# Optimization experiments

Hardware: AMD Instinct MI355X
Metric: run time of the kernel (lower is better)

## Reference

```python
import jax, jax.numpy as jnp
import numpy as np

N = 131072      # total nodes in batch
D = 128         # input_dim
K_EXP = 1024    # input_dim * num_conv_kernels
H = 512         # cluster_model_hidden_dim
NG = 4          # number of groups (sub-models)
F_SEG = 8192    # fine clusters (global_max_pool segments)
G_SEG = 32      # coarse graphs (InstanceNorm segments)
C = 16          # node_num_classes
EPS = 1e-5      # InstanceNorm eps


def setup_inputs() -> dict:
    key = jax.random.key(0)
    ks = jax.random.split(key, 8)
    x = jax.random.normal(ks[0], (N, D), jnp.float32)
    # disjoint partition of node indices into NG groups (gather/scatter dispatch)
    group_indices = jax.random.permutation(ks[1], N).reshape(NG, N // NG)
    # sorted segment ids, every segment non-empty
    pool_cluster_fine = (jnp.arange(N) // (N // F_SEG)).astype(jnp.int32)
    batch_cluster_coarse = (jnp.arange(F_SEG) // (F_SEG // G_SEG)).astype(jnp.int32)
    # per-group NodeModel params: expand D -> K_EXP, relu, project -> H
    W1 = jax.random.normal(ks[2], (NG, D, K_EXP), jnp.float32) * (1.0 / np.sqrt(D))
    b1 = jnp.zeros((NG, K_EXP), jnp.float32)
    W2 = jax.random.normal(ks[3], (NG, K_EXP, H), jnp.float32) * (1.0 / np.sqrt(K_EXP))
    b2 = jnp.zeros((NG, H), jnp.float32)
    # classifier (glorot weight, zero bias)
    w_out = jax.random.normal(ks[4], (H, C), jnp.float32) * np.sqrt(2.0 / (H + C))
    b_out = jnp.zeros((C,), jnp.float32)
    return {"x": x, "group_indices": group_indices,
            "pool_cluster_fine": pool_cluster_fine,
            "batch_cluster_coarse": batch_cluster_coarse,
            "W1": W1, "b1": b1, "W2": W2, "b2": b2,
            "w_out": w_out, "b_out": b_out}


def reference(x, group_indices, pool_cluster_fine, batch_cluster_coarse,
              W1, b1, W2, b2, w_out, b_out):
    # per-group gather -> sub-model -> scatter (vectorized over groups)
    xg = x[group_indices]                                   # [NG, N/NG, D]
    h = jax.nn.relu(jnp.einsum('gnd,gdk->gnk', xg, W1) + b1[:, None, :])
    og = jnp.einsum('gnk,gkh->gnh', h, W2) + b2[:, None, :]  # [NG, N/NG, H]
    new_feat = jnp.zeros((x.shape[0], H), x.dtype).at[group_indices.reshape(-1)].set(
        og.reshape(-1, H))                                   # [N, H]
    # global_max_pool over fine clusters
    emb = jax.ops.segment_max(new_feat, pool_cluster_fine,
                              num_segments=F_SEG, indices_are_sorted=True)  # [F, H]
    # PyG InstanceNorm(affine=False): per coarse-graph, per-channel standardization
    ones = jnp.ones((F_SEG, 1), emb.dtype)
    cnt = jax.ops.segment_sum(ones, batch_cluster_coarse,
                              num_segments=G_SEG, indices_are_sorted=True)  # [G,1]
    mean = jax.ops.segment_sum(emb, batch_cluster_coarse,
                               num_segments=G_SEG, indices_are_sorted=True) / cnt
    var = jax.ops.segment_sum(emb * emb, batch_cluster_coarse,
                              num_segments=G_SEG, indices_are_sorted=True) / cnt - mean ** 2
    normed = (emb - mean[batch_cluster_coarse]) * jax.lax.rsqrt(var[batch_cluster_coarse] + EPS)
    # dropout is identity in eval mode; classifier
    logits = normed @ w_out + b_out                          # [F, C]
    return logits
```

## Files before the change

kernel.cpp:

```cpp
#include <hip/hip_runtime.h>
#include <stdint.h>

typedef __bf16 bf16;
typedef bf16 bf16x8 __attribute__((ext_vector_type(8)));
typedef float f32x4 __attribute__((ext_vector_type(4)));

#define N_NODES 131072
#define D_IN    128
#define KEXP    1024
#define H_DIM   512
#define NGRP    4
#define NPG     32768
#define F_SEG   8192
#define G_SEG   32
#define C_OUT   16

typedef const __attribute__((address_space(1))) void* gas_t;
typedef __attribute__((address_space(3))) void* las_t;
__device__ __forceinline__ void cp16_async(const bf16* g, bf16* l) {
    __builtin_amdgcn_global_load_lds((gas_t)g, (las_t)l, 16, 0, 0);
}

__global__ void convert_weights(const float* __restrict__ W1,
                                const float* __restrict__ W2,
                                bf16* __restrict__ W1F,
                                bf16* __restrict__ W2F)
{
    int t = blockIdx.x * 256 + threadIdx.x;
    if (t < 65536) {
        int slot = t & 63, f = (t >> 6) & 7, kc = (t >> 9) & 31, g = t >> 14;
        int ks = f >> 1, nt = f & 1, quad = slot >> 4, ln = slot & 15;
        int k = kc * 32 + nt * 16 + ln;
        const float* src = W1 + ((size_t)(g * 128 + ks * 32 + quad * 8)) * 1024 + k;
        bf16x8 v;
        #pragma unroll
        for (int j = 0; j < 8; ++j) v[j] = (bf16)src[(size_t)j * 1024];
        *(bf16x8*)(W1F + (size_t)t * 8) = v;
    } else {
        int u = t - 65536;
        if (u < 262144) {
            int slot = u & 63, f = (u >> 6) & 15, kc = (u >> 10) & 31;
            int n0t2 = (u >> 15) & 1, g = u >> 16;
            int quad = slot >> 4, ln = slot & 15;
            int k = kc * 32 + quad * 8;
            int n = n0t2 * 256 + f * 16 + ln;
            const float* src = W2 + ((size_t)(g * 1024 + k)) * 512 + n;
            bf16x8 v;
            #pragma unroll
            for (int j = 0; j < 8; ++j) v[j] = (bf16)src[(size_t)j * 512];
            *(bf16x8*)(W2F + (size_t)u * 8) = v;
        }
    }
}

__global__ __launch_bounds__(256, 2)
void mlp_kernel(const float* __restrict__ x,
                const int*   __restrict__ gidx,
                const bf16*  __restrict__ W1F,
                const float* __restrict__ b1,
                const bf16*  __restrict__ W2F,
                const float* __restrict__ b2,
                bf16*        __restrict__ NF)
{
    __shared__ __align__(16) bf16 sW1[2][4096];
    __shared__ __align__(16) bf16 sW2[2][8192];
    __shared__ __align__(16) bf16 sH[4096];

    const int tid  = threadIdx.x;
    const int bid  = blockIdx.x;
    const int g    = bid >> 9;
    const int rem  = bid & 511;
    const int m0   = (rem >> 1) * 128;
    const int n0t2 = rem & 1;

    const int wave = tid >> 6;
    const int lane = tid & 63;
    const int quad = lane >> 4;
    const int ln   = lane & 15;

    const int*  gI  = gidx + g * NPG + m0;
    const bf16* W1g = W1F + (size_t)g * 131072;
    const bf16* W2g = W2F + (size_t)(g * 2 + n0t2) * 262144;
    const float* b1g = b1 + g * KEXP;
    const float* b2g = b2 + g * H_DIM + n0t2 * 256;

    bf16x8 xf[8];
    #pragma unroll
    for (int i = 0; i < 8; ++i) {
        int row  = wave * 32 + (i >> 2) * 16 + ln;
        int node = gI[row];
        const float* src = x + (size_t)node * D_IN + (i & 3) * 32 + quad * 8;
        float4 a = *(const float4*)src;
        float4 b = *(const float4*)(src + 4);
        bf16x8 v;
        v[0] = (bf16)a.x; v[1] = (bf16)a.y; v[2] = (bf16)a.z; v[3] = (bf16)a.w;
        v[4] = (bf16)b.x; v[5] = (bf16)b.y; v[6] = (bf16)b.z; v[7] = (bf16)b.w;
        xf[i] = v;
    }

    f32x4 acc2[2][16];
    #pragma unroll
    for (int a = 0; a < 2; ++a)
        #pragma unroll
        for (int b = 0; b < 16; ++b)
            acc2[a][b] = (f32x4){0.f, 0.f, 0.f, 0.f};

    #pragma unroll
    for (int r = 0; r < 2; ++r) {
        int c = r * 4 + wave;
        cp16_async(W1g + c * 512 + lane * 8, sW1[0] + c * 512);
    }
    #pragma unroll
    for (int r = 0; r < 4; ++r) {
        int c = r * 4 + wave;
        cp16_async(W2g + c * 512 + lane * 8, sW2[0] + c * 512);
    }

    #pragma unroll 1
    for (int kc = 0; kc < 32; ++kc) {
        __syncthreads();

        {
            int nkc = (kc + 1) & 31;
            const bf16* w1src = W1g + (size_t)nkc * 4096;
            const bf16* w2src = W2g + (size_t)nkc * 8192;
            bf16* d1 = sW1[(kc + 1) & 1];
            bf16* d2 = sW2[(kc + 1) & 1];
            #pragma unroll
            for (int r = 0; r < 2; ++r) {
                int c = r * 4 + wave;
                cp16_async(w1src + c * 512 + lane * 8, d1 + c * 512);
            }
            #pragma unroll
            for (int r = 0; r < 4; ++r) {
                int c = r * 4 + wave;
                cp16_async(w2src + c * 512 + lane * 8, d2 + c * 512);
            }
        }
        const bf16* w1buf = sW1[kc & 1];
        const bf16* w2buf = sW2[kc & 1];

        float bias_v[2];
        #pragma unroll
        for (int nt = 0; nt < 2; ++nt)
            bias_v[nt] = b1g[kc * 32 + nt * 16 + ln];

        f32x4 acc1[2][2];
        #pragma unroll
        for (int a = 0; a < 2; ++a)
            #pragma unroll
            for (int b = 0; b < 2; ++b)
                acc1[a][b] = (f32x4){0.f, 0.f, 0.f, 0.f};

        #pragma unroll
        for (int ks = 0; ks < 4; ++ks) {
            #pragma unroll
            for (int nt = 0; nt < 2; ++nt) {
                bf16x8 bfr = *(const bf16x8*)(w1buf + ((ks * 2 + nt) * 64 + lane) * 8);
                #pragma unroll
                for (int mt = 0; mt < 2; ++mt)
                    acc1[mt][nt] = __builtin_amdgcn_mfma_f32_16x16x32_bf16(
                        xf[mt * 4 + ks], bfr, acc1[mt][nt], 0, 0, 0);
            }
        }

        #pragma unroll
        for (int nt = 0; nt < 2; ++nt) {
            float bias = bias_v[nt];
            int base = wave * 1024 + (nt * 2 + (ln >> 3)) * 128
                     + (quad * 4) * 8 + (ln & 7);
            #pragma unroll
            for (int mt = 0; mt < 2; ++mt) {
                int fb = base + mt * 512;
                #pragma unroll
                for (int reg = 0; reg < 4; ++reg) {
                    float v = acc1[mt][nt][reg] + bias;
                    sH[fb + reg * 8] = (bf16)fmaxf(v, 0.f);
                }
            }
        }

        bf16x8 a2[2];
        #pragma unroll
        for (int mt = 0; mt < 2; ++mt)
            a2[mt] = *(const bf16x8*)(sH + wave * 1024 + mt * 512 + lane * 8);
        #pragma unroll
        for (int nt = 0; nt < 16; ++nt) {
            bf16x8 bb = *(const bf16x8*)(w2buf + (nt * 64 + lane) * 8);
            #pragma unroll
            for (int mt = 0; mt < 2; ++mt)
                acc2[mt][nt] = __builtin_amdgcn_mfma_f32_16x16x32_bf16(
                    a2[mt], bb, acc2[mt][nt], 0, 0, 0);
        }
    }

    float b2v[16];
    #pragma unroll
    for (int nt = 0; nt < 16; ++nt) b2v[nt] = b2g[nt * 16 + ln];

    #pragma unroll
    for (int mt = 0; mt < 2; ++mt)
        #pragma unroll
        for (int reg = 0; reg < 4; ++reg) {
            int row  = wave * 32 + mt * 16 + quad * 4 + reg;
            int node = gI[row];
            bf16* dst = NF + (size_t)node * H_DIM + n0t2 * 256;
            #pragma unroll
            for (int nt = 0; nt < 16; ++nt)
                dst[nt * 16 + ln] = (bf16)(acc2[mt][nt][reg] + b2v[nt]);
        }
}

__global__ void pool_kernel(const bf16* __restrict__ NF, float* __restrict__ EMB)
{
    int t  = blockIdx.x * 256 + threadIdx.x;
    int f  = t >> 8;
    int hp = (t & 255) * 2;
    const uint32_t* src = (const uint32_t*)NF;
    size_t base = (size_t)f * 4096 + (hp >> 1);
    float lo = -INFINITY, hi = -INFINITY;
    #pragma unroll
    for (int r = 0; r < 16; ++r) {
        uint32_t v = src[base + (size_t)r * 256];
        lo = fmaxf(lo, __uint_as_float(v << 16));
        hi = fmaxf(hi, __uint_as_float(v & 0xffff0000u));
    }
    *(float2*)(EMB + (size_t)f * 512 + hp) = make_float2(lo, hi);
}

__global__ void stats_kernel(const float* __restrict__ EMB,
                             float* __restrict__ MEAN,
                             float* __restrict__ RSIG)
{
    int gc = blockIdx.x;
    int ch = blockIdx.y * 128 + threadIdx.x;
    const float* p = EMB + (size_t)gc * 256 * 512 + ch;
    float s = 0.f, ss = 0.f;
    #pragma unroll 4
    for (int r = 0; r < 256; ++r) {
        float v = p[(size_t)r * 512];
        s += v; ss += v * v;
    }
    float mean = s * (1.f / 256.f);
    float var  = ss * (1.f / 256.f) - mean * mean;
    MEAN[gc * 512 + ch] = mean;
    RSIG[gc * 512 + ch] = rsqrtf(var + 1e-5f);
}

__global__ __launch_bounds__(256)
void classifier_kernel(const float* __restrict__ EMB,
                       const float* __restrict__ MEAN,
                       const float* __restrict__ RSIG,
                       const float* __restrict__ w_out,
                       const float* __restrict__ b_out,
                       float* __restrict__ out)
{
    __shared__ float sW[512 * 16];
    __shared__ float sE[16 * 513];
    int t  = threadIdx.x;
    int f0 = blockIdx.x * 16;
    int gc = f0 >> 8;

    #pragma unroll
    for (int it = 0; it < 8; ++it) {
        int i = (it * 256 + t) * 4;
        *(float4*)(sW + i) = *(const float4*)(w_out + i);
    }
    #pragma unroll
    for (int it = 0; it < 32; ++it) {
        int i  = it * 256 + t;
        int fr = i >> 9;
        int h  = i & 511;
        float v = EMB[(size_t)(f0 + fr) * 512 + h];
        sE[fr * 513 + h] = (v - MEAN[gc * 512 + h]) * RSIG[gc * 512 + h];
    }
    __syncthreads();

    int fr = t >> 4;
    int c  = t & 15;
    float acc = b_out[c];
    #pragma unroll 8
    for (int h = 0; h < 512; ++h)
        acc += sE[fr * 513 + h] * sW[h * 16 + c];
    out[(size_t)(f0 + fr) * 16 + c] = acc;
}

extern "C" void kernel_launch(void* const* d_in, const int* in_sizes, int n_in,
                              void* d_out, int out_size, void* d_ws, size_t ws_size,
                              hipStream_t stream)
{
    const float* x     = (const float*)d_in[0];
    const int*   gidx  = (const int*)d_in[1];
    const float* W1    = (const float*)d_in[4];
    const float* b1    = (const float*)d_in[5];
    const float* W2    = (const float*)d_in[6];
    const float* b2    = (const float*)d_in[7];
    const float* w_out = (const float*)d_in[8];
    const float* b_out = (const float*)d_in[9];
    float* out = (float*)d_out;

    char* w = (char*)d_ws;
    bf16* W1F = (bf16*)w;  w += (size_t)NGRP * KEXP * D_IN * 2;
    bf16* W2F = (bf16*)w;  w += (size_t)NGRP * H_DIM * KEXP * 2;
    bf16* NF  = (bf16*)w;  w += (size_t)N_NODES * H_DIM * 2;
    float* EMB  = (float*)w; w += (size_t)F_SEG * H_DIM * 4;
    float* MEAN = (float*)w; w += (size_t)G_SEG * H_DIM * 4;
    float* RSIG = (float*)w; w += (size_t)G_SEG * H_DIM * 4;

    convert_weights<<<1280, 256, 0, stream>>>(W1, W2, W1F, W2F);
    mlp_kernel<<<2048, 256, 0, stream>>>(x, gidx, W1F, b1, W2F, b2, NF);
    pool_kernel<<<8192, 256, 0, stream>>>(NF, EMB);
    stats_kernel<<<dim3(32, 4), 128, 0, stream>>>(EMB, MEAN, RSIG);
    classifier_kernel<<<512, 256, 0, stream>>>(EMB, MEAN, RSIG, w_out, b_out, out);
}
```

Baseline: 387.5 us.

## Fuse segment max-pool into MLP epilogue via atomicMax on order-preserving encoded floats

Removes the bf16 NF intermediate and the separate pool kernel. The MLP epilogue now does atomicMax directly into an fp32 embedding buffer, using a sign-flipping float-to-uint encoding so integer max matches float max. The embedding buffer is zeroed inside the weight-conversion kernel. The second GEMM is also re-tiled so each wave covers all 128 rows against its own 64 output columns, with an extra barrier because sH is now shared across waves. This trades a large NF write and re-read for many global atomics (16 nodes per segment hit the same address) and an added sync per k-step.

```diff
diff --git a/kernel.cpp b/kernel.cpp
--- a/kernel.cpp
+++ b/kernel.cpp
@@ -21,10 +21,20 @@
     __builtin_amdgcn_global_load_lds((gas_t)g, (las_t)l, 16, 0, 0);
 }
 
+__device__ __forceinline__ uint32_t enc_f32(float f) {
+    uint32_t b = __float_as_uint(f);
+    return (b & 0x80000000u) ? ~b : (b | 0x80000000u);
+}
+__device__ __forceinline__ float dec_f32(uint32_t k) {
+    uint32_t b = (k & 0x80000000u) ? (k & 0x7FFFFFFFu) : ~k;
+    return __uint_as_float(b);
+}
+
 __global__ void convert_weights(const float* __restrict__ W1,
                                 const float* __restrict__ W2,
                                 bf16* __restrict__ W1F,
-                                bf16* __restrict__ W2F)
+                                bf16* __restrict__ W2F,
+                                uint32_t* __restrict__ EMBu)
 {
     int t = blockIdx.x * 256 + threadIdx.x;
     if (t < 65536) {
@@ -36,20 +46,21 @@
         #pragma unroll
         for (int j = 0; j < 8; ++j) v[j] = (bf16)src[(size_t)j * 1024];
         *(bf16x8*)(W1F + (size_t)t * 8) = v;
+    } else if (t < 327680) {
+        int u = t - 65536;
+        int slot = u & 63, f = (u >> 6) & 15, kc = (u >> 10) & 31;
+        int n0t2 = (u >> 15) & 1, g = u >> 16;
+        int quad = slot >> 4, ln = slot & 15;
+        int k = kc * 32 + quad * 8;
+        int n = n0t2 * 256 + f * 16 + ln;
+        const float* src = W2 + ((size_t)(g * 1024 + k)) * 512 + n;
+        bf16x8 v;
+        #pragma unroll
+        for (int j = 0; j < 8; ++j) v[j] = (bf16)src[(size_t)j * 512];
+        *(bf16x8*)(W2F + (size_t)u * 8) = v;
     } else {
-        int u = t - 65536;
-        if (u < 262144) {
-            int slot = u & 63, f = (u >> 6) & 15, kc = (u >> 10) & 31;
-            int n0t2 = (u >> 15) & 1, g = u >> 16;
-            int quad = slot >> 4, ln = slot & 15;
-            int k = kc * 32 + quad * 8;
-            int n = n0t2 * 256 + f * 16 + ln;
-            const float* src = W2 + ((size_t)(g * 1024 + k)) * 512 + n;
-            bf16x8 v;
-            #pragma unroll
-            for (int j = 0; j < 8; ++j) v[j] = (bf16)src[(size_t)j * 512];
-            *(bf16x8*)(W2F + (size_t)u * 8) = v;
-        }
+        int z = t - 327680;
+        if (z < F_SEG * H_DIM) EMBu[z] = 0u;
     }
 }
 
@@ -60,7 +71,7 @@
                 const float* __restrict__ b1,
                 const bf16*  __restrict__ W2F,
                 const float* __restrict__ b2,
-                bf16*        __restrict__ NF)
+                uint32_t*    __restrict__ EMBu)
 {
     __shared__ __align__(16) bf16 sW1[2][4096];
     __shared__ __align__(16) bf16 sW2[2][8192];
@@ -98,11 +109,11 @@
         xf[i] = v;
     }
 
-    f32x4 acc2[2][16];
-    #pragma unroll
-    for (int a = 0; a < 2; ++a)
-        #pragma unroll
-        for (int b = 0; b < 16; ++b)
+    f32x4 acc2[8][4];
+    #pragma unroll
+    for (int a = 0; a < 8; ++a)
+        #pragma unroll
+        for (int b = 0; b < 4; ++b)
             acc2[a][b] = (f32x4){0.f, 0.f, 0.f, 0.f};
 
     #pragma unroll
@@ -120,26 +131,7 @@
     for (int kc = 0; kc < 32; ++kc) {
         __syncthreads();
 
-        {
-            int nkc = (kc + 1) & 31;
-            const bf16* w1src = W1g + (size_t)nkc * 4096;
-            const bf16* w2src = W2g + (size_t)nkc * 8192;
-            bf16* d1 = sW1[(kc + 1) & 1];
-            bf16* d2 = sW2[(kc + 1) & 1];
-            #pragma unroll
-            for (int r = 0; r < 2; ++r) {
-                int c = r * 4 + wave;
-                cp16_async(w1src + c * 512 + lane * 8, d1 + c * 512);
-            }
-            #pragma unroll
-            for (int r = 0; r < 4; ++r) {
-                int c = r * 4 + wave;
-                cp16_async(w2src + c * 512 + lane * 8, d2 + c * 512);
-            }
-        }
         const bf16* w1buf = sW1[kc & 1];
-        const bf16* w2buf = sW2[kc & 1];
-
         float bias_v[2];
         #pragma unroll
         for (int nt = 0; nt < 2; ++nt)
@@ -168,7 +160,7 @@
         for (int nt = 0; nt < 2; ++nt) {
             float bias = bias_v[nt];
             int base = wave * 1024 + (nt * 2 + (ln >> 3)) * 128
-                     + (quad * 4) * 8 + (ln & 7);
+                     + quad * 32 + (ln & 7);
             #pragma unroll
             for (int mt = 0; mt < 2; ++mt) {
                 int fb = base + mt * 512;
@@ -180,65 +172,72 @@
             }
         }
 
-        bf16x8 a2[2];
-        #pragma unroll
-        for (int mt = 0; mt < 2; ++mt)
-            a2[mt] = *(const bf16x8*)(sH + wave * 1024 + mt * 512 + lane * 8);
-        #pragma unroll
-        for (int nt = 0; nt < 16; ++nt) {
-            bf16x8 bb = *(const bf16x8*)(w2buf + (nt * 64 + lane) * 8);
-            #pragma unroll
-            for (int mt = 0; mt < 2; ++mt)
+        __syncthreads();
+
+        {
+            int nkc = (kc + 1) & 31;
+            const bf16* w1src = W1g + (size_t)nkc * 4096;
+            const bf16* w2src = W2g + (size_t)nkc * 8192;
+            bf16* d1 = sW1[(kc + 1) & 1];
+            bf16* d2 = sW2[(kc + 1) & 1];
+            #pragma unroll
+            for (int r = 0; r < 2; ++r) {
+                int c = r * 4 + wave;
+                cp16_async(w1src + c * 512 + lane * 8, d1 + c * 512);
+            }
+            #pragma unroll
+            for (int r = 0; r < 4; ++r) {
+                int c = r * 4 + wave;
+                cp16_async(w2src + c * 512 + lane * 8, d2 + c * 512);
+            }
+        }
+
+        const bf16* w2buf = sW2[kc & 1];
+        bf16x8 bb[4];
+        #pragma unroll
+        for (int nt = 0; nt < 4; ++nt)
+            bb[nt] = *(const bf16x8*)(w2buf + ((wave * 4 + nt) * 64 + lane) * 8);
+        #pragma unroll
+        for (int mt = 0; mt < 8; ++mt) {
+            bf16x8 a2 = *(const bf16x8*)(sH + (mt * 64 + lane) * 8);
+            #pragma unroll
+            for (int nt = 0; nt < 4; ++nt)
                 acc2[mt][nt] = __builtin_amdgcn_mfma_f32_16x16x32_bf16(
-                    a2[mt], bb, acc2[mt][nt], 0, 0, 0);
-        }
-    }
-
-    float b2v[16];
-    #pragma unroll
-    for (int nt = 0; nt < 16; ++nt) b2v[nt] = b2g[nt * 16 + ln];
-
-    #pragma unroll
-    for (int mt = 0; mt < 2; ++mt)
+                    a2, bb[nt], acc2[mt][nt], 0, 0, 0);
+        }
+    }
+
+    float b2v[4];
+    #pragma unroll
+    for (int nt = 0; nt < 4; ++nt) b2v[nt] = b2g[wave * 64 + nt * 16 + ln];
+
+    #pragma unroll
+    for (int mt = 0; mt < 8; ++mt)
         #pragma unroll
         for (int reg = 0; reg < 4; ++reg) {
-            int row  = wave * 32 + mt * 16 + quad * 4 + reg;
+            int row  = mt * 16 + quad * 4 + reg;
             int node = gI[row];
-            bf16* dst = NF + (size_t)node * H_DIM + n0t2 * 256;
-            #pragma unroll
-            for (int nt = 0; nt < 16; ++nt)
-                dst[nt * 16 + ln] = (bf16)(acc2[mt][nt][reg] + b2v[nt]);
-        }
-}
-
-__global__ void pool_kernel(const bf16* __restrict__ NF, float* __restrict__ EMB)
-{
-    int t  = blockIdx.x * 256 + threadIdx.x;
-    int f  = t >> 8;
-    int hp = (t & 255) * 2;
-    const uint32_t* src = (const uint32_t*)NF;
-    size_t base = (size_t)f * 4096 + (hp >> 1);
-    float lo = -INFINITY, hi = -INFINITY;
-    #pragma unroll
-    for (int r = 0; r < 16; ++r) {
-        uint32_t v = src[base + (size_t)r * 256];
-        lo = fmaxf(lo, __uint_as_float(v << 16));
-        hi = fmaxf(hi, __uint_as_float(v & 0xffff0000u));
-    }
-    *(float2*)(EMB + (size_t)f * 512 + hp) = make_float2(lo, hi);
-}
-
-__global__ void stats_kernel(const float* __restrict__ EMB,
+            uint32_t* dst = EMBu + (size_t)(node >> 4) * H_DIM
+                          + n0t2 * 256 + wave * 64;
+            #pragma unroll
+            for (int nt = 0; nt < 4; ++nt) {
+                float v = acc2[mt][nt][reg] + b2v[nt];
+                atomicMax(dst + nt * 16 + ln, enc_f32(v));
+            }
+        }
+}
+
+__global__ void stats_kernel(const uint32_t* __restrict__ EMBu,
                              float* __restrict__ MEAN,
                              float* __restrict__ RSIG)
 {
     int gc = blockIdx.x;
     int ch = blockIdx.y * 128 + threadIdx.x;
-    const float* p = EMB + (size_t)gc * 256 * 512 + ch;
+    const uint32_t* p = EMBu + (size_t)gc * 256 * 512 + ch;
     float s = 0.f, ss = 0.f;
     #pragma unroll 4
     for (int r = 0; r < 256; ++r) {
-        float v = p[(size_t)r * 512];
+        float v = dec_f32(p[(size_t)r * 512]);
         s += v; ss += v * v;
     }
     float mean = s * (1.f / 256.f);
@@ -248,7 +247,7 @@
 }
 
 __global__ __launch_bounds__(256)
-void classifier_kernel(const float* __restrict__ EMB,
+void classifier_kernel(const uint32_t* __restrict__ EMBu,
                        const float* __restrict__ MEAN,
                        const float* __restrict__ RSIG,
                        const float* __restrict__ w_out,
@@ -271,7 +270,7 @@
         int i  = it * 256 + t;
         int fr = i >> 9;
         int h  = i & 511;
-        float v = EMB[(size_t)(f0 + fr) * 512 + h];
+        float v = dec_f32(EMBu[(size_t)(f0 + fr) * 512 + h]);
         sE[fr * 513 + h] = (v - MEAN[gc * 512 + h]) * RSIG[gc * 512 + h];
     }
     __syncthreads();
@@ -302,14 +301,12 @@
     char* w = (char*)d_ws;
     bf16* W1F = (bf16*)w;  w += (size_t)NGRP * KEXP * D_IN * 2;
     bf16* W2F = (bf16*)w;  w += (size_t)NGRP * H_DIM * KEXP * 2;
-    bf16* NF  = (bf16*)w;  w += (size_t)N_NODES * H_DIM * 2;
-    float* EMB  = (float*)w; w += (size_t)F_SEG * H_DIM * 4;
+    uint32_t* EMBu = (uint32_t*)w; w += (size_t)F_SEG * H_DIM * 4;
     float* MEAN = (float*)w; w += (size_t)G_SEG * H_DIM * 4;
     float* RSIG = (float*)w; w += (size_t)G_SEG * H_DIM * 4;
 
-    convert_weights<<<1280, 256, 0, stream>>>(W1, W2, W1F, W2F);
-    mlp_kernel<<<2048, 256, 0, stream>>>(x, gidx, W1F, b1, W2F, b2, NF);
-    pool_kernel<<<8192, 256, 0, stream>>>(NF, EMB);
-    stats_kernel<<<dim3(32, 4), 128, 0, stream>>>(EMB, MEAN, RSIG);
-    classifier_kernel<<<512, 256, 0, stream>>>(EMB, MEAN, RSIG, w_out, b_out, out);
-}
+    convert_weights<<<17664, 256, 0, stream>>>(W1, W2, W1F, W2F, EMBu);
+    mlp_kernel<<<2048, 256, 0, stream>>>(x, gidx, W1F, b1, W2F, b2, EMBu);
+    stats_kernel<<<dim3(32, 4), 128, 0, stream>>>(EMBu, MEAN, RSIG);
+    classifier_kernel<<<512, 256, 0, stream>>>(EMBu, MEAN, RSIG, w_out, b_out, out);
+}
```

Result: slower. 446.3 us (+15.2%).

## Retile second GEMM as 2x2 wave grid and vectorize max-pool loads

Applied to the files above, without the earlier changes.

The second GEMM in the MLP kernel is re-tiled so each wave computes a 64x128 output tile (4 M-tiles by 8 N-tiles) instead of 32x256. Every wave now reads the shared hidden activations written by the other waves, so a barrier is added after the sH writes, and the W1 prefetch is moved after that barrier so it cannot overwrite buffers still being read. The point is to cut LDS traffic for W2 fragments per MFMA, at the cost of an extra barrier per k-chunk and different register pressure. Separately, the pool kernel loads 16-byte vectors of 8 bf16 channels per thread and launches a quarter as many blocks.

```diff
diff --git a/kernel.cpp b/kernel.cpp
--- a/kernel.cpp
+++ b/kernel.cpp
@@ -77,12 +77,13 @@
     const int lane = tid & 63;
     const int quad = lane >> 4;
     const int ln   = lane & 15;
+    const int mg   = wave >> 1;
+    const int ng   = wave & 1;
 
     const int*  gI  = gidx + g * NPG + m0;
     const bf16* W1g = W1F + (size_t)g * 131072;
     const bf16* W2g = W2F + (size_t)(g * 2 + n0t2) * 262144;
     const float* b1g = b1 + g * KEXP;
-    const float* b2g = b2 + g * H_DIM + n0t2 * 256;
 
     bf16x8 xf[8];
     #pragma unroll
@@ -98,11 +99,11 @@
         xf[i] = v;
     }
 
-    f32x4 acc2[2][16];
-    #pragma unroll
-    for (int a = 0; a < 2; ++a)
-        #pragma unroll
-        for (int b = 0; b < 16; ++b)
+    f32x4 acc2[4][8];
+    #pragma unroll
+    for (int a = 0; a < 4; ++a)
+        #pragma unroll
+        for (int b = 0; b < 8; ++b)
             acc2[a][b] = (f32x4){0.f, 0.f, 0.f, 0.f};
 
     #pragma unroll
@@ -122,24 +123,16 @@
 
         {
             int nkc = (kc + 1) & 31;
-            const bf16* w1src = W1g + (size_t)nkc * 4096;
             const bf16* w2src = W2g + (size_t)nkc * 8192;
-            bf16* d1 = sW1[(kc + 1) & 1];
             bf16* d2 = sW2[(kc + 1) & 1];
-            #pragma unroll
-            for (int r = 0; r < 2; ++r) {
-                int c = r * 4 + wave;
-                cp16_async(w1src + c * 512 + lane * 8, d1 + c * 512);
-            }
             #pragma unroll
             for (int r = 0; r < 4; ++r) {
                 int c = r * 4 + wave;
                 cp16_async(w2src + c * 512 + lane * 8, d2 + c * 512);
             }
         }
+
         const bf16* w1buf = sW1[kc & 1];
-        const bf16* w2buf = sW2[kc & 1];
-
         float bias_v[2];
         #pragma unroll
         for (int nt = 0; nt < 2; ++nt)
@@ -168,7 +161,7 @@
         for (int nt = 0; nt < 2; ++nt) {
             float bias = bias_v[nt];
             int base = wave * 1024 + (nt * 2 + (ln >> 3)) * 128
-                     + (quad * 4) * 8 + (ln & 7);
+                     + quad * 32 + (ln & 7);
             #pragma unroll
             for (int mt = 0; mt < 2; ++mt) {
                 int fb = base + mt * 512;
@@ -180,33 +173,48 @@
             }
         }
 
-        bf16x8 a2[2];
-        #pragma unroll
-        for (int mt = 0; mt < 2; ++mt)
-            a2[mt] = *(const bf16x8*)(sH + wave * 1024 + mt * 512 + lane * 8);
-        #pragma unroll
-        for (int nt = 0; nt < 16; ++nt) {
-            bf16x8 bb = *(const bf16x8*)(w2buf + (nt * 64 + lane) * 8);
-            #pragma unroll
-            for (int mt = 0; mt < 2; ++mt)
+        __syncthreads();
+
+        {
+            int nkc = (kc + 1) & 31;
+            const bf16* w1src = W1g + (size_t)nkc * 4096;
+            bf16* d1 = sW1[(kc + 1) & 1];
+            #pragma unroll
+            for (int r = 0; r < 2; ++r) {
+                int c = r * 4 + wave;
+                cp16_async(w1src + c * 512 + lane * 8, d1 + c * 512);
+            }
+        }
+
+        const bf16* w2buf = sW2[kc & 1];
+        bf16x8 bb[8];
+        #pragma unroll
+        for (int nt = 0; nt < 8; ++nt)
+            bb[nt] = *(const bf16x8*)(w2buf + ((ng * 8 + nt) * 64 + lane) * 8);
+        #pragma unroll
+        for (int mt = 0; mt < 4; ++mt) {
+            bf16x8 a2 = *(const bf16x8*)(sH + ((mg * 4 + mt) * 64 + lane) * 8);
+            #pragma unroll
+            for (int nt = 0; nt < 8; ++nt)
                 acc2[mt][nt] = __builtin_amdgcn_mfma_f32_16x16x32_bf16(
-                    a2[mt], bb, acc2[mt][nt], 0, 0, 0);
-        }
-    }
-
-    float b2v[16];
-    #pragma unroll
-    for (int nt = 0; nt < 16; ++nt) b2v[nt] = b2g[nt * 16 + ln];
-
-    #pragma unroll
-    for (int mt = 0; mt < 2; ++mt)
+                    a2, bb[nt], acc2[mt][nt], 0, 0, 0);
+        }
+    }
+
+    const float* b2g = b2 + g * H_DIM + n0t2 * 256 + ng * 128;
+    float b2v[8];
+    #pragma unroll
+    for (int nt = 0; nt < 8; ++nt) b2v[nt] = b2g[nt * 16 + ln];
+
+    #pragma unroll
+    for (int mt = 0; mt < 4; ++mt)
         #pragma unroll
         for (int reg = 0; reg < 4; ++reg) {
-            int row  = wave * 32 + mt * 16 + quad * 4 + reg;
+            int row  = mg * 64 + mt * 16 + quad * 4 + reg;
             int node = gI[row];
-            bf16* dst = NF + (size_t)node * H_DIM + n0t2 * 256;
-            #pragma unroll
-            for (int nt = 0; nt < 16; ++nt)
+            bf16* dst = NF + (size_t)node * H_DIM + n0t2 * 256 + ng * 128;
+            #pragma unroll
+            for (int nt = 0; nt < 8; ++nt)
                 dst[nt * 16 + ln] = (bf16)(acc2[mt][nt][reg] + b2v[nt]);
         }
 }
@@ -214,18 +222,25 @@
 __global__ void pool_kernel(const bf16* __restrict__ NF, float* __restrict__ EMB)
 {
     int t  = blockIdx.x * 256 + threadIdx.x;
-    int f  = t >> 8;
-    int hp = (t & 255) * 2;
-    const uint32_t* src = (const uint32_t*)NF;
-    size_t base = (size_t)f * 4096 + (hp >> 1);
-    float lo = -INFINITY, hi = -INFINITY;
+    int f  = t >> 6;
+    int c8 = (t & 63) * 8;
+    const uint4* src = (const uint4*)(NF + (size_t)f * 16 * 512 + c8);
+    float m[8];
+    #pragma unroll
+    for (int i = 0; i < 8; ++i) m[i] = -INFINITY;
     #pragma unroll
     for (int r = 0; r < 16; ++r) {
-        uint32_t v = src[base + (size_t)r * 256];
-        lo = fmaxf(lo, __uint_as_float(v << 16));
-        hi = fmaxf(hi, __uint_as_float(v & 0xffff0000u));
-    }
-    *(float2*)(EMB + (size_t)f * 512 + hp) = make_float2(lo, hi);
+        uint4 v = src[(size_t)r * 64];
+        uint32_t w[4] = {v.x, v.y, v.z, v.w};
+        #pragma unroll
+        for (int i = 0; i < 4; ++i) {
+            m[2*i]   = fmaxf(m[2*i],   __uint_as_float(w[i] << 16));
+            m[2*i+1] = fmaxf(m[2*i+1], __uint_as_float(w[i] & 0xffff0000u));
+        }
+    }
+    float* dst = EMB + (size_t)f * 512 + c8;
+    *(float4*)dst       = make_float4(m[0], m[1], m[2], m[3]);
+    *(float4*)(dst + 4) = make_float4(m[4], m[5], m[6], m[7]);
 }
 
 __global__ void stats_kernel(const float* __restrict__ EMB,
@@ -309,7 +324,7 @@
 
     convert_weights<<<1280, 256, 0, stream>>>(W1, W2, W1F, W2F);
     mlp_kernel<<<2048, 256, 0, stream>>>(x, gidx, W1F, b1, W2F, b2, NF);
-    pool_kernel<<<8192, 256, 0, stream>>>(NF, EMB);
+    pool_kernel<<<2048, 256, 0, stream>>>(NF, EMB);
     stats_kernel<<<dim3(32, 4), 128, 0, stream>>>(EMB, MEAN, RSIG);
     classifier_kernel<<<512, 256, 0, stream>>>(EMB, MEAN, RSIG, w_out, b_out, out);
 }
```

Result: faster. 375.6 us (-3.1%).
